# Kernel tuning notes

Hardware: AMD Instinct MI355X
Metric: run time of the kernel (lower is better)

## Reference

```python
import jax, jax.numpy as jnp
import numpy as np
from jax import lax

K = 3       # kernel_conv
STRIDE = 1
PAD = 1


def setup_inputs() -> dict:
    key = jax.random.key(0)
    ks = jax.random.split(key, 11)
    b, n, H, W = 8, 64, 128, 128
    m = 64
    kk = K * K
    return {
        "x": jax.random.normal(ks[0], (b, n, H, W), jnp.float32),
        "atw1": jax.random.uniform(ks[1], (b, kk, H, W), jnp.float32),  # sigmoid-range attention1 output
        "weight": jax.random.normal(ks[2], (m, n, K, K), jnp.float32) * 0.05,
        "a2_w1": jax.random.normal(ks[3], (kk, n), jnp.float32) * 0.1,
        "a2_b1": jax.random.normal(ks[4], (kk,), jnp.float32) * 0.1,
        "a2_w2": jax.random.normal(ks[5], (kk, kk), jnp.float32) * 0.1,
        "a2_b2": jax.random.normal(ks[6], (kk,), jnp.float32) * 0.1,
        "a3_w1": jax.random.normal(ks[7], (m, n), jnp.float32) * 0.1,
        "a3_b1": jax.random.normal(ks[8], (m,), jnp.float32) * 0.1,
        "a3_w2": jax.random.normal(ks[9], (m, m), jnp.float32) * 0.1,
        "a3_b2": jax.random.normal(ks[10], (m,), jnp.float32) * 0.1,
    }


def reference(x, atw1, weight, a2_w1, a2_b1, a2_w2, a2_b2, a3_w1, a3_b1, a3_w2, a3_b2):
    b, n, H, W = x.shape
    m = weight.shape[0]
    kk = K * K
    n_H = 1 + (H + 2 * PAD - K) // STRIDE
    n_W = 1 + (W + 2 * PAD - K) // STRIDE
    P = n_H * n_W

    # F.unfold(x, k, stride, padding): [b, n*k*k, P] with channel-major ordering (c, kh, kw)
    patches = lax.conv_general_dilated_patches(
        x, (K, K), (STRIDE, STRIDE), [(PAD, PAD), (PAD, PAD)])  # [b, n*kk, n_H, n_W]
    kx = patches.reshape(b, n, kk, P)

    # attention2: global avg pool + two 1x1 convs -> per-batch per-tap ratio [b, kk]
    g = x.mean(axis=(2, 3))                                   # [b, n]
    ratio = jax.nn.relu(g @ a2_w1.T + a2_b1) @ a2_w2.T + a2_b2  # [b, kk]

    # per-pixel per-tap weight (broadcast over input channels, as the torch repeat/view does)
    a = atw1.reshape(b, kk, P) * ratio[:, :, None]            # [b, kk, P]
    wx = kx * a[:, None, :, :]                                # [b, n, kk, P]

    # dynamic-weighted im2col matmul with static conv weight
    w = weight.reshape(m, n, kk)
    y = jnp.einsum('bctp,mct->bmp', wx, w)                    # [b, m, P]

    # attention3 bias: global avg pool + two 1x1 convs -> [b, m]
    bias = jax.nn.relu(g @ a3_w1.T + a3_b1) @ a3_w2.T + a3_b2
    y = y + bias[:, :, None]

    # F.fold with kernel 1 is a reshape back to the spatial grid
    return y.reshape(b, m, n_H, n_W)
```

## Files before the change

kernel.cpp:

```cpp
#include <hip/hip_runtime.h>

typedef __attribute__((ext_vector_type(8))) short short8;
typedef __attribute__((ext_vector_type(4))) float f32x4;

#define HH 128
#define WW 128
#define TW 16
#define TH 4
#define HALOW 18
#define HALOH 6
#define NPIX (HALOW * HALOH)
#define XSB (NPIX * 128)
#define NA (9 * TH * TW)

__device__ inline unsigned short f2bf(float f) {
    unsigned int u = __builtin_bit_cast(unsigned int, f);
    u += 0x7fffu + ((u >> 16) & 1u);
    return (unsigned short)(u >> 16);
}

__global__ __launch_bounds__(256) void prep_kernel(
    const float* __restrict__ x, const float* __restrict__ wgt,
    unsigned short* __restrict__ xT, float* __restrict__ partials,
    unsigned short* __restrict__ W3) {
    const int id = blockIdx.x;
    const int tid = threadIdx.x;
    {
        int i = id * 256 + tid;
        if (i < 64 * 64 * 9) {
            int j = i & 7, rest = i >> 3;
            int m = rest & 63; rest >>= 6;
            int lk = rest & 3; rest >>= 2;
            int ks = rest & 1, t = rest >> 1;
            int c = ks * 32 + lk * 8 + j;
            W3[i] = f2bf(wgt[(m * 64 + c) * 9 + t]);
        }
    }
    const int b = id & 7, pt = id >> 3;
    const int p0 = pt * 64;
    __shared__ unsigned int lt[64 * 33];
    __shared__ float red[8][32][2];

    const int px = tid & 63, cp0 = tid >> 6;
    const float* xb = x + (size_t)b * 64 * (HH * WW) + p0 + px;
    #pragma unroll
    for (int i = 0; i < 8; ++i) {
        int cp = cp0 + 4 * i;
        float v0 = xb[(size_t)(2 * cp) * (HH * WW)];
        float v1 = xb[(size_t)(2 * cp + 1) * (HH * WW)];
        lt[px * 33 + cp] = (unsigned)f2bf(v0) | ((unsigned)f2bf(v1) << 16);
    }
    __syncthreads();
    #pragma unroll
    for (int it = 0; it < 2; ++it) {
        int idx = it * 256 + tid;
        int p = idx >> 3, ch = idx & 7;
        int o = p * 33 + ch * 4;
        uint4 v = make_uint4(lt[o], lt[o + 1], lt[o + 2], lt[o + 3]);
        *(uint4*)(xT + ((size_t)(b * (HH * WW) + p0 + p) * 64 + ch * 8)) = v;
    }
    {
        int cp = tid & 31, grp = tid >> 5;
        float s0 = 0.f, s1 = 0.f;
        #pragma unroll
        for (int j2 = 0; j2 < 8; ++j2) {
            unsigned u = lt[(grp * 8 + j2) * 33 + cp];
            s0 += __builtin_bit_cast(float, u << 16);
            s1 += __builtin_bit_cast(float, u & 0xffff0000u);
        }
        red[grp][cp][0] = s0;
        red[grp][cp][1] = s1;
    }
    __syncthreads();
    if (tid < 64) {
        float s = 0.f;
        #pragma unroll
        for (int g2 = 0; g2 < 8; ++g2) s += red[g2][tid >> 1][tid & 1];
        partials[(size_t)(b * 256 + pt) * 64 + tid] = s;
    }
}

__global__ __launch_bounds__(256) void mlp_kernel(
    const float* __restrict__ partials,
    const float* __restrict__ a2w1, const float* __restrict__ a2b1,
    const float* __restrict__ a2w2, const float* __restrict__ a2b2,
    const float* __restrict__ a3w1, const float* __restrict__ a3b1,
    const float* __restrict__ a3w2, const float* __restrict__ a3b2,
    float* __restrict__ ratio, float* __restrict__ bias) {
    int b = blockIdx.x;
    int tid = threadIdx.x;
    int t = tid & 63, is = tid >> 6;
    float s = 0.f;
    #pragma unroll 8
    for (int k = 0; k < 64; ++k)
        s += partials[(size_t)(b * 256 + is + 4 * k) * 64 + t];
    __shared__ float rb[4][64];
    __shared__ float gs[64], h2[9], h3[64];
    rb[is][t] = s;
    __syncthreads();
    if (tid < 64)
        gs[t] = (rb[0][t] + rb[1][t] + rb[2][t] + rb[3][t]) * (1.f / (HH * WW));
    __syncthreads();
    if (tid < 64) {
        float s3 = 0.f;
        #pragma unroll 8
        for (int i = 0; i < 64; ++i) s3 += gs[i] * a3w1[t * 64 + i];
        h3[t] = fmaxf(s3 + a3b1[t], 0.f);
        if (t < 9) {
            float s2 = 0.f;
            #pragma unroll 8
            for (int i = 0; i < 64; ++i) s2 += gs[i] * a2w1[t * 64 + i];
            h2[t] = fmaxf(s2 + a2b1[t], 0.f);
        }
    }
    __syncthreads();
    if (tid < 64) {
        float o = 0.f;
        #pragma unroll 8
        for (int i = 0; i < 64; ++i) o += h3[i] * a3w2[t * 64 + i];
        bias[b * 64 + t] = o + a3b2[t];
        if (t < 9) {
            float r = 0.f;
            #pragma unroll
            for (int i = 0; i < 9; ++i) r += h2[i] * a2w2[t * 9 + i];
            ratio[b * 9 + t] = r + a2b2[t];
        }
    }
}

__global__ __launch_bounds__(256, 2) void main_kernel(
    const unsigned short* __restrict__ xT, const float* __restrict__ atw1,
    const unsigned short* __restrict__ W3, const float* __restrict__ ratio,
    const float* __restrict__ bias, float* __restrict__ out) {
    const int id = blockIdx.x;
    const int b = id & 7;
    const int j = id >> 3;
    const int tid = threadIdx.x;
    const int lane = tid & 63;
    const int wtile = tid >> 6;
    const int lm = lane & 15;
    const int lk = lane >> 4;

    __shared__ char xsc[2][XSB];
    __shared__ float alds[2][NA];

    short8 wfrag[9][2];
    {
        const short8* W3v = (const short8*)W3;
        #pragma unroll
        for (int t = 0; t < 9; ++t)
            #pragma unroll
            for (int ks = 0; ks < 2; ++ks)
                wfrag[t][ks] = W3v[(((t * 2 + ks) * 4 + lk) * 64) + wtile * 16 + lm];
    }
    float biasr[4];
    #pragma unroll
    for (int q = 0; q < 4; ++q) biasr[q] = bias[b * 64 + wtile * 16 + lk * 4 + q];

    const unsigned short* xb = xT + (size_t)b * (HH * WW) * 64;
    const float* ab = atw1 + (size_t)b * 9 * (HH * WW);
    const float* rg = ratio + b * 9;
    float* ob = out + (size_t)b * 64 * (HH * WW);

    uint4 sx[4];
    float sa[3];

    auto LOADT = [&](int task) {
        const int py0 = (task >> 3) * TH, px0 = (task & 7) * TW;
        #pragma unroll
        for (int i = 0; i < 4; ++i) {
            int idx = i * 256 + tid;
            uint4 v = make_uint4(0u, 0u, 0u, 0u);
            if (idx < NPIX * 8) {
                int pix = idx >> 3, ch = idx & 7;
                int yy = pix / HALOW;
                int xx = pix - yy * HALOW;
                int gy = py0 + yy - 1, gx = px0 + xx - 1;
                if (gy >= 0 && gy < HH && gx >= 0 && gx < WW)
                    v = *(const uint4*)(xb + ((size_t)(gy * WW + gx) * 64 + ch * 8));
            }
            sx[i] = v;
        }
        #pragma unroll
        for (int i = 0; i < 3; ++i) {
            int idx = i * 256 + tid;
            float v = 0.f;
            if (idx < NA) {
                int t = idx >> 6, rem = idx & 63;
                int rr = rem >> 4, cc = rem & 15;
                v = ab[(size_t)t * (HH * WW) + (py0 + rr) * WW + px0 + cc] * rg[t];
            }
            sa[i] = v;
        }
    };
    auto DSWRITE = [&](int bi) {
        #pragma unroll
        for (int i = 0; i < 4; ++i) {
            int idx = i * 256 + tid;
            if (idx < NPIX * 8) {
                int pix = idx >> 3, ch = idx & 7;
                *(uint4*)(&xsc[bi][pix * 128 + ((ch * 16) ^ ((pix & 7) << 4))]) = sx[i];
            }
        }
        #pragma unroll
        for (int i = 0; i < 3; ++i) {
            int idx = i * 256 + tid;
            if (idx < NA) alds[bi][idx] = sa[i];
        }
    };

    LOADT(j * 4);
    DSWRITE(0);
    __syncthreads();

    #pragma unroll 1
    for (int it = 0; it < 4; ++it) {
        if (it < 3) LOADT(j * 4 + it + 1);

        const int task = j * 4 + it;
        const int py0 = (task >> 3) * TH, px0 = (task & 7) * TW;
        const char* xs = xsc[it & 1];
        const float* al = alds[it & 1];

        #pragma unroll
        for (int g2 = 0; g2 < 2; ++g2) {
            const int r0 = g2 * 2;
            float av[2][9];
            #pragma unroll
            for (int rr = 0; rr < 2; ++rr)
                #pragma unroll
                for (int t = 0; t < 9; ++t) av[rr][t] = al[t * 64 + (r0 + rr) * 16 + lm];

            f32x4 yac[2];
            #pragma unroll
            for (int rr = 0; rr < 2; ++rr) yac[rr] = (f32x4){0.f, 0.f, 0.f, 0.f};

            #pragma unroll
            for (int hl = 0; hl < 4; ++hl) {
                const int pixr = (r0 + hl) * HALOW + lm;
                short8 bf[3][2];
                #pragma unroll
                for (int dx = 0; dx < 3; ++dx) {
                    const int pix = pixr + dx;
                    const int sw = (pix & 7) << 4;
                    const char* bp2 = xs + pix * 128;
                    #pragma unroll
                    for (int ks = 0; ks < 2; ++ks)
                        bf[dx][ks] = __builtin_bit_cast(short8,
                            *(const uint4*)(bp2 + ((ks * 64 + lk * 16) ^ sw)));
                }
                #pragma unroll
                for (int dy = 0; dy < 3; ++dy) {
                    const int r = hl - dy;
                    if (r < 0 || r > 1) continue;
                    #pragma unroll
                    for (int dx = 0; dx < 3; ++dx) {
                        const int t = dy * 3 + dx;
                        f32x4 z = {0.f, 0.f, 0.f, 0.f};
                        z = __builtin_amdgcn_mfma_f32_16x16x32_bf16(wfrag[t][0], bf[dx][0], z, 0, 0, 0);
                        z = __builtin_amdgcn_mfma_f32_16x16x32_bf16(wfrag[t][1], bf[dx][1], z, 0, 0, 0);
                        #pragma unroll
                        for (int q = 0; q < 4; ++q) yac[r][q] = fmaf(av[r][t], z[q], yac[r][q]);
                    }
                }
            }
            #pragma unroll
            for (int rr = 0; rr < 2; ++rr) {
                const int pyg = py0 + r0 + rr;
                #pragma unroll
                for (int q = 0; q < 4; ++q) {
                    int m = wtile * 16 + lk * 4 + q;
                    ob[((size_t)m * HH + pyg) * WW + px0 + lm] = yac[rr][q] + biasr[q];
                }
            }
        }

        if (it < 3) DSWRITE((it + 1) & 1);
        __syncthreads();
    }
}

extern "C" void kernel_launch(void* const* d_in, const int* in_sizes, int n_in,
                              void* d_out, int out_size, void* d_ws, size_t ws_size,
                              hipStream_t stream) {
    const float* x    = (const float*)d_in[0];
    const float* atw1 = (const float*)d_in[1];
    const float* wgt  = (const float*)d_in[2];
    const float* a2w1 = (const float*)d_in[3];
    const float* a2b1 = (const float*)d_in[4];
    const float* a2w2 = (const float*)d_in[5];
    const float* a2b2 = (const float*)d_in[6];
    const float* a3w1 = (const float*)d_in[7];
    const float* a3b1 = (const float*)d_in[8];
    const float* a3w2 = (const float*)d_in[9];
    const float* a3b2 = (const float*)d_in[10];
    float* out = (float*)d_out;

    float* ws = (float*)d_ws;
    float* ratio = ws;
    float* bias  = ws + 128;
    unsigned short* W3 = (unsigned short*)(ws + 1024);
    float* partials = ws + 19456;
    unsigned short* xT = (unsigned short*)(ws + 150528);

    prep_kernel<<<dim3(2048), dim3(256), 0, stream>>>(x, wgt, xT, partials, W3);
    mlp_kernel<<<dim3(8), dim3(256), 0, stream>>>(partials, a2w1, a2b1, a2w2, a2b2,
                                                  a3w1, a3b1, a3w2, a3b2, ratio, bias);
    main_kernel<<<dim3(512), dim3(256), 0, stream>>>(xT, atw1, W3, ratio, bias, out);
}
```

Measured before the change: 41.83 us.

## Split warps over output-channel pairs and row halves to reuse B fragments

Each warp now computes two 16-channel output tiles for two output rows, instead of one channel tile for all four rows. Every shared-memory B fragment load then feeds two MFMA pairs, which halves LDS read traffic per MFMA. Warps also no longer loop over both row groups, and the attention scalars are read from LDS at the point of use instead of being preloaded. The cost is doubled weight-fragment registers (36 short8), which may pressure the two-blocks-per-SM occupancy target.

```diff
diff --git a/kernel.cpp b/kernel.cpp
--- a/kernel.cpp
+++ b/kernel.cpp
@@ -137,25 +137,33 @@
     const int j = id >> 3;
     const int tid = threadIdx.x;
     const int lane = tid & 63;
-    const int wtile = tid >> 6;
+    const int w = tid >> 6;
+    const int mh = w >> 1;
+    const int rh = w & 1;
     const int lm = lane & 15;
     const int lk = lane >> 4;
 
     __shared__ char xsc[2][XSB];
     __shared__ float alds[2][NA];
 
-    short8 wfrag[9][2];
+    short8 wfrag[9][2][2];
     {
         const short8* W3v = (const short8*)W3;
         #pragma unroll
         for (int t = 0; t < 9; ++t)
             #pragma unroll
             for (int ks = 0; ks < 2; ++ks)
-                wfrag[t][ks] = W3v[(((t * 2 + ks) * 4 + lk) * 64) + wtile * 16 + lm];
-    }
-    float biasr[4];
+                #pragma unroll
+                for (int mt = 0; mt < 2; ++mt)
+                    wfrag[t][ks][mt] =
+                        W3v[(((t * 2 + ks) * 4 + lk) * 64) + (mh * 2 + mt) * 16 + lm];
+    }
+    float biasr[2][4];
     #pragma unroll
-    for (int q = 0; q < 4; ++q) biasr[q] = bias[b * 64 + wtile * 16 + lk * 4 + q];
+    for (int mt = 0; mt < 2; ++mt)
+        #pragma unroll
+        for (int q = 0; q < 4; ++q)
+            biasr[mt][q] = bias[b * 64 + (mh * 2 + mt) * 16 + lk * 4 + q];
 
     const unsigned short* xb = xT + (size_t)b * (HH * WW) * 64;
     const float* ab = atw1 + (size_t)b * 9 * (HH * WW);
@@ -222,57 +230,58 @@
         const char* xs = xsc[it & 1];
         const float* al = alds[it & 1];
 
-        #pragma unroll
-        for (int g2 = 0; g2 < 2; ++g2) {
-            const int r0 = g2 * 2;
-            float av[2][9];
-            #pragma unroll
-            for (int rr = 0; rr < 2; ++rr)
+        f32x4 yac[2][2];
+        #pragma unroll
+        for (int r = 0; r < 2; ++r)
+            #pragma unroll
+            for (int mt = 0; mt < 2; ++mt) yac[r][mt] = (f32x4){0.f, 0.f, 0.f, 0.f};
+
+        #pragma unroll
+        for (int hl = 0; hl < 4; ++hl) {
+            const int pixr = (rh * 2 + hl) * HALOW + lm;
+            short8 bf[3][2];
+            #pragma unroll
+            for (int dx = 0; dx < 3; ++dx) {
+                const int pix = pixr + dx;
+                const int sw = (pix & 7) << 4;
+                const char* bp2 = xs + pix * 128;
                 #pragma unroll
-                for (int t = 0; t < 9; ++t) av[rr][t] = al[t * 64 + (r0 + rr) * 16 + lm];
-
-            f32x4 yac[2];
-            #pragma unroll
-            for (int rr = 0; rr < 2; ++rr) yac[rr] = (f32x4){0.f, 0.f, 0.f, 0.f};
-
-            #pragma unroll
-            for (int hl = 0; hl < 4; ++hl) {
-                const int pixr = (r0 + hl) * HALOW + lm;
-                short8 bf[3][2];
+                for (int ks = 0; ks < 2; ++ks)
+                    bf[dx][ks] = __builtin_bit_cast(short8,
+                        *(const uint4*)(bp2 + ((ks * 64 + lk * 16) ^ sw)));
+            }
+            #pragma unroll
+            for (int dy = 0; dy < 3; ++dy) {
+                const int r = hl - dy;
+                if (r < 0 || r > 1) continue;
                 #pragma unroll
                 for (int dx = 0; dx < 3; ++dx) {
-                    const int pix = pixr + dx;
-                    const int sw = (pix & 7) << 4;
-                    const char* bp2 = xs + pix * 128;
+                    const int t = dy * 3 + dx;
+                    f32x4 z0 = {0.f, 0.f, 0.f, 0.f};
+                    f32x4 z1 = {0.f, 0.f, 0.f, 0.f};
+                    z0 = __builtin_amdgcn_mfma_f32_16x16x32_bf16(wfrag[t][0][0], bf[dx][0], z0, 0, 0, 0);
+                    z0 = __builtin_amdgcn_mfma_f32_16x16x32_bf16(wfrag[t][1][0], bf[dx][1], z0, 0, 0, 0);
+                    z1 = __builtin_amdgcn_mfma_f32_16x16x32_bf16(wfrag[t][0][1], bf[dx][0], z1, 0, 0, 0);
+                    z1 = __builtin_amdgcn_mfma_f32_16x16x32_bf16(wfrag[t][1][1], bf[dx][1], z1, 0, 0, 0);
+                    const float a = al[t * 64 + (rh * 2 + r) * 16 + lm];
                     #pragma unroll
-                    for (int ks = 0; ks < 2; ++ks)
-                        bf[dx][ks] = __builtin_bit_cast(short8,
-                            *(const uint4*)(bp2 + ((ks * 64 + lk * 16) ^ sw)));
-                }
-                #pragma unroll
-                for (int dy = 0; dy < 3; ++dy) {
-                    const int r = hl - dy;
-                    if (r < 0 || r > 1) continue;
-                    #pragma unroll
-                    for (int dx = 0; dx < 3; ++dx) {
-                        const int t = dy * 3 + dx;
-                        f32x4 z = {0.f, 0.f, 0.f, 0.f};
-                        z = __builtin_amdgcn_mfma_f32_16x16x32_bf16(wfrag[t][0], bf[dx][0], z, 0, 0, 0);
-                        z = __builtin_amdgcn_mfma_f32_16x16x32_bf16(wfrag[t][1], bf[dx][1], z, 0, 0, 0);
-                        #pragma unroll
-                        for (int q = 0; q < 4; ++q) yac[r][q] = fmaf(av[r][t], z[q], yac[r][q]);
+                    for (int q = 0; q < 4; ++q) {
+                        yac[r][0][q] = fmaf(a, z0[q], yac[r][0][q]);
+                        yac[r][1][q] = fmaf(a, z1[q], yac[r][1][q]);
                     }
                 }
             }
-            #pragma unroll
-            for (int rr = 0; rr < 2; ++rr) {
-                const int pyg = py0 + r0 + rr;
+        }
+        #pragma unroll
+        for (int r = 0; r < 2; ++r) {
+            const int pyg = py0 + rh * 2 + r;
+            #pragma unroll
+            for (int mt = 0; mt < 2; ++mt)
                 #pragma unroll
                 for (int q = 0; q < 4; ++q) {
-                    int m = wtile * 16 + lk * 4 + q;
-                    ob[((size_t)m * HH + pyg) * WW + px0 + lm] = yac[rr][q] + biasr[q];
+                    int m = (mh * 2 + mt) * 16 + lk * 4 + q;
+                    ob[((size_t)m * HH + pyg) * WW + px0 + lm] = yac[r][mt][q] + biasr[mt][q];
                 }
-            }
         }
 
         if (it < 3) DSWRITE((it + 1) & 1);
```

Result: slower. 62.57 us (+49.6%).

## Stage halo tiles via direct global-to-LDS loads with zero-page padding

Applied to the files above, without the earlier changes.

Replaces the register-staged prefetch (global load into VGPRs, then ds_write after compute) with global_load_lds DMA straight into shared memory. Out-of-bounds pixels read from a small zeroed page that prep_kernel writes. The XOR swizzle moves from the LDS address to the global source address, and the ratio multiply moves from staging into the attention read. This frees registers and removes the separate LDS write pass. In exchange, the LDS buffers grow to fixed padded sizes, and correctness depends on the async loads completing before the barrier.

```diff
diff --git a/kernel.cpp b/kernel.cpp
--- a/kernel.cpp
+++ b/kernel.cpp
@@ -10,8 +10,10 @@
 #define HALOW 18
 #define HALOH 6
 #define NPIX (HALOW * HALOH)
-#define XSB (NPIX * 128)
 #define NA (9 * TH * TW)
+
+typedef __attribute__((address_space(1))) const unsigned int glds_src_t;
+typedef __attribute__((address_space(3))) unsigned int glds_dst_t;
 
 __device__ inline unsigned short f2bf(float f) {
     unsigned int u = __builtin_bit_cast(unsigned int, f);
@@ -22,9 +24,10 @@
 __global__ __launch_bounds__(256) void prep_kernel(
     const float* __restrict__ x, const float* __restrict__ wgt,
     unsigned short* __restrict__ xT, float* __restrict__ partials,
-    unsigned short* __restrict__ W3) {
+    unsigned short* __restrict__ W3, float* __restrict__ zpage) {
     const int id = blockIdx.x;
     const int tid = threadIdx.x;
+    if (id == 0 && tid < 32) zpage[tid] = 0.f;
     {
         int i = id * 256 + tid;
         if (i < 64 * 64 * 9) {
@@ -131,7 +134,8 @@
 __global__ __launch_bounds__(256, 2) void main_kernel(
     const unsigned short* __restrict__ xT, const float* __restrict__ atw1,
     const unsigned short* __restrict__ W3, const float* __restrict__ ratio,
-    const float* __restrict__ bias, float* __restrict__ out) {
+    const float* __restrict__ bias, float* __restrict__ out,
+    const float* __restrict__ zpage) {
     const int id = blockIdx.x;
     const int b = id & 7;
     const int j = id >> 3;
@@ -141,8 +145,8 @@
     const int lm = lane & 15;
     const int lk = lane >> 4;
 
-    __shared__ char xsc[2][XSB];
-    __shared__ float alds[2][NA];
+    __shared__ char xsc[2][16384];
+    __shared__ float alds[2][768];
 
     short8 wfrag[9][2];
     {
@@ -153,69 +157,54 @@
             for (int ks = 0; ks < 2; ++ks)
                 wfrag[t][ks] = W3v[(((t * 2 + ks) * 4 + lk) * 64) + wtile * 16 + lm];
     }
+    float rat[9];
+    #pragma unroll
+    for (int t = 0; t < 9; ++t) rat[t] = ratio[b * 9 + t];
     float biasr[4];
     #pragma unroll
     for (int q = 0; q < 4; ++q) biasr[q] = bias[b * 64 + wtile * 16 + lk * 4 + q];
 
-    const unsigned short* xb = xT + (size_t)b * (HH * WW) * 64;
+    const char* xbb = (const char*)(xT + (size_t)b * (HH * WW) * 64);
     const float* ab = atw1 + (size_t)b * 9 * (HH * WW);
-    const float* rg = ratio + b * 9;
     float* ob = out + (size_t)b * 64 * (HH * WW);
-
-    uint4 sx[4];
-    float sa[3];
-
-    auto LOADT = [&](int task) {
+    const char* zp = (const char*)zpage;
+
+    auto STAGE = [&](int bi, int task) {
         const int py0 = (task >> 3) * TH, px0 = (task & 7) * TW;
         #pragma unroll
         for (int i = 0; i < 4; ++i) {
             int idx = i * 256 + tid;
-            uint4 v = make_uint4(0u, 0u, 0u, 0u);
-            if (idx < NPIX * 8) {
-                int pix = idx >> 3, ch = idx & 7;
-                int yy = pix / HALOW;
-                int xx = pix - yy * HALOW;
-                int gy = py0 + yy - 1, gx = px0 + xx - 1;
-                if (gy >= 0 && gy < HH && gx >= 0 && gx < WW)
-                    v = *(const uint4*)(xb + ((size_t)(gy * WW + gx) * 64 + ch * 8));
-            }
-            sx[i] = v;
+            int pix = idx >> 3, ch = idx & 7;
+            int yy = pix / HALOW;
+            int xx = pix - yy * HALOW;
+            int gy = py0 + yy - 1, gx = px0 + xx - 1;
+            bool ok = (pix < NPIX) && (gy >= 0) && (gy < HH) && (gx >= 0) && (gx < WW);
+            const char* src = ok
+                ? xbb + (((size_t)(gy * WW + gx)) << 7) + ((ch * 16) ^ ((pix & 7) << 4))
+                : zp;
+            char* dst = &xsc[bi][(i * 256 + wtile * 64) * 16];
+            __builtin_amdgcn_global_load_lds((glds_src_t*)src, (glds_dst_t*)dst, 16, 0, 0);
         }
         #pragma unroll
         for (int i = 0; i < 3; ++i) {
             int idx = i * 256 + tid;
-            float v = 0.f;
-            if (idx < NA) {
-                int t = idx >> 6, rem = idx & 63;
-                int rr = rem >> 4, cc = rem & 15;
-                v = ab[(size_t)t * (HH * WW) + (py0 + rr) * WW + px0 + cc] * rg[t];
-            }
-            sa[i] = v;
+            int t = idx >> 6, rem = idx & 63;
+            int rr = rem >> 4, cc = rem & 15;
+            bool ok = idx < NA;
+            const char* src = ok
+                ? (const char*)(ab + (size_t)t * (HH * WW) + (py0 + rr) * WW + px0 + cc)
+                : zp;
+            float* dst = &alds[bi][i * 256 + wtile * 64];
+            __builtin_amdgcn_global_load_lds((glds_src_t*)src, (glds_dst_t*)dst, 4, 0, 0);
         }
     };
-    auto DSWRITE = [&](int bi) {
-        #pragma unroll
-        for (int i = 0; i < 4; ++i) {
-            int idx = i * 256 + tid;
-            if (idx < NPIX * 8) {
-                int pix = idx >> 3, ch = idx & 7;
-                *(uint4*)(&xsc[bi][pix * 128 + ((ch * 16) ^ ((pix & 7) << 4))]) = sx[i];
-            }
-        }
-        #pragma unroll
-        for (int i = 0; i < 3; ++i) {
-            int idx = i * 256 + tid;
-            if (idx < NA) alds[bi][idx] = sa[i];
-        }
-    };
-
-    LOADT(j * 4);
-    DSWRITE(0);
+
+    STAGE(0, j * 4);
     __syncthreads();
 
     #pragma unroll 1
     for (int it = 0; it < 4; ++it) {
-        if (it < 3) LOADT(j * 4 + it + 1);
+        if (it < 3) STAGE((it + 1) & 1, j * 4 + it + 1);
 
         const int task = j * 4 + it;
         const int py0 = (task >> 3) * TH, px0 = (task & 7) * TW;
@@ -229,7 +218,8 @@
             #pragma unroll
             for (int rr = 0; rr < 2; ++rr)
                 #pragma unroll
-                for (int t = 0; t < 9; ++t) av[rr][t] = al[t * 64 + (r0 + rr) * 16 + lm];
+                for (int t = 0; t < 9; ++t)
+                    av[rr][t] = al[t * 64 + (r0 + rr) * 16 + lm] * rat[t];
 
             f32x4 yac[2];
             #pragma unroll
@@ -275,7 +265,6 @@
             }
         }
 
-        if (it < 3) DSWRITE((it + 1) & 1);
         __syncthreads();
     }
 }
@@ -299,12 +288,13 @@
     float* ws = (float*)d_ws;
     float* ratio = ws;
     float* bias  = ws + 128;
+    float* zpage = ws + 640;
     unsigned short* W3 = (unsigned short*)(ws + 1024);
     float* partials = ws + 19456;
     unsigned short* xT = (unsigned short*)(ws + 150528);
 
-    prep_kernel<<<dim3(2048), dim3(256), 0, stream>>>(x, wgt, xT, partials, W3);
+    prep_kernel<<<dim3(2048), dim3(256), 0, stream>>>(x, wgt, xT, partials, W3, zpage);
     mlp_kernel<<<dim3(8), dim3(256), 0, stream>>>(partials, a2w1, a2b1, a2w2, a2b2,
                                                   a3w1, a3b1, a3w2, a3b2, ratio, bias);
-    main_kernel<<<dim3(512), dim3(256), 0, stream>>>(xT, atw1, W3, ratio, bias, out);
-}
+    main_kernel<<<dim3(512), dim3(256), 0, stream>>>(xT, atw1, W3, ratio, bias, out, zpage);
+}
```

New measurement: 40.51 us. 1.03x faster.
